# Kernel tuning notes

Hardware: AMD Instinct MI355X
Metric: run time of the kernel (lower is better)

Reference implementation:

```python
import jax, jax.numpy as jnp
import numpy as np


def setup_inputs() -> dict:
    key = jax.random.key(0)
    kx, kq = jax.random.split(key)
    x = jax.random.normal(kx, (64, 1024, 1024), dtype=jnp.float32)
    # K=16 quantization points, sorted (the kernel assumes a fixed ordered set)
    qpoints = jnp.sort(jax.random.uniform(kq, (16,), dtype=jnp.float32,
                                          minval=-1.5, maxval=1.5))
    return {"x": x, "qpoints": qpoints}


def reference(x, qpoints):
    # Nearest-qpoint quantize without materializing an (N, K) distance matrix.
    # searchsorted gives, for each element, the index of the first qpoint >= x;
    # the nearest point is either that one or its left neighbor.
    K = qpoints.shape[0]
    idx = jnp.searchsorted(qpoints, x)            # in [0, K]
    lo = qpoints[jnp.clip(idx - 1, 0, K - 1)]     # left neighbor
    hi = qpoints[jnp.clip(idx, 0, K - 1)]         # right neighbor
    out = jnp.where(jnp.abs(x - lo) <= jnp.abs(x - hi), lo, hi)
    return out
```

## Files before the change

### kernel.cpp

```cpp
#include <hip/hip_runtime.h>


__device__ __forceinline__ float rfl(float v) {
    return __int_as_float(__builtin_amdgcn_readfirstlane(__float_as_int(v)));
}

__device__ __forceinline__ float quant1(float xv, const float qp[16]) {
    float hi = qp[15];
#pragma unroll
    for (int k = 14; k >= 0; --k) hi = (qp[k] >= xv) ? qp[k] : hi;
    float lo = qp[0];
#pragma unroll
    for (int k = 1; k < 16; ++k) lo = (qp[k] < xv) ? qp[k] : lo;
    return (fabsf(xv - lo) <= fabsf(xv - hi)) ? lo : hi;
}

__global__ __launch_bounds__(256) void qquant_vec4(
    const float4* __restrict__ x, const float* __restrict__ q,
    float4* __restrict__ out, int n4) {
    const float4* q4 = (const float4*)q;
    float4 q0 = q4[0], q1 = q4[1], q2 = q4[2], q3 = q4[3];
    float qp[16] = {rfl(q0.x), rfl(q0.y), rfl(q0.z), rfl(q0.w),
                    rfl(q1.x), rfl(q1.y), rfl(q1.z), rfl(q1.w),
                    rfl(q2.x), rfl(q2.y), rfl(q2.z), rfl(q2.w),
                    rfl(q3.x), rfl(q3.y), rfl(q3.z), rfl(q3.w)};

    int stride = gridDim.x * blockDim.x;
    for (int i = blockIdx.x * blockDim.x + threadIdx.x; i < n4; i += stride) {
        float4 v = x[i];
        float4 r;
        r.x = quant1(v.x, qp);
        r.y = quant1(v.y, qp);
        r.z = quant1(v.z, qp);
        r.w = quant1(v.w, qp);
        out[i] = r;
    }
}

__global__ void qquant_tail(const float* __restrict__ x,
                            const float* __restrict__ q,
                            float* __restrict__ out, int start, int n) {
    int i = start + threadIdx.x;
    if (i >= n) return;
    float qp[16];
#pragma unroll
    for (int k = 0; k < 16; ++k) qp[k] = q[k];
    out[i] = quant1(x[i], qp);
}

extern "C" void kernel_launch(void* const* d_in, const int* in_sizes, int n_in,
                              void* d_out, int out_size, void* d_ws, size_t ws_size,
                              hipStream_t stream) {
    const float* x = (const float*)d_in[0];
    const float* q = (const float*)d_in[1];
    float* out = (float*)d_out;
    int n = in_sizes[0];

    int n4 = n >> 2;
    if (n4 > 0) {
        int blocks = (n4 + 255) / 256;
        if (blocks > 8192) blocks = 8192;
        qquant_vec4<<<blocks, 256, 0, stream>>>((const float4*)x, q,
                                                (float4*)out, n4);
    }
    int rem = n & 3;
    if (rem > 0) {
        qquant_tail<<<1, 64, 0, stream>>>(x, q, out, n4 << 2, n);
    }
}
```

Measured before the change: 443.1 us.

## Precompute exact midpoint thresholds and quantize with a single compare chain

Adds a small setup kernel that binary-searches, in ordered-float space, the exact decision threshold between each pair of adjacent qpoints under the reference tie rule, and stores the thresholds in workspace. The main kernel then picks the output with one 15-step compare/select chain per element instead of two 15-step chains plus distance arithmetic. It also switches global loads and stores to nontemporal. This cuts ALU work per element at the cost of an extra tiny kernel launch and a dependence on workspace being available. The kernel is likely near memory-bound, which would limit the benefit.

```diff
diff --git a/kernel.cpp b/kernel.cpp
--- a/kernel.cpp
+++ b/kernel.cpp
@@ -1,8 +1,70 @@
 #include <hip/hip_runtime.h>
 
 
+typedef float f32x4 __attribute__((ext_vector_type(4)));
+
 __device__ __forceinline__ float rfl(float v) {
     return __int_as_float(__builtin_amdgcn_readfirstlane(__float_as_int(v)));
+}
+
+__device__ __forceinline__ unsigned f2o(float f) {
+    unsigned b = __float_as_uint(f);
+    return (b & 0x80000000u) ? ~b : (b | 0x80000000u);
+}
+__device__ __forceinline__ float o2f(unsigned o) {
+    unsigned b = (o & 0x80000000u) ? (o ^ 0x80000000u) : ~o;
+    return __uint_as_float(b);
+}
+
+__global__ void qthresh_setup(const float* __restrict__ q,
+                              float* __restrict__ t) {
+    int k = threadIdx.x;
+    if (k > 15) return;
+    if (k == 15) { t[15] = __uint_as_float(0x7f800000u); return; }
+    float lo = q[k], hi = q[k + 1];
+    unsigned a = f2o(lo), b = f2o(hi);
+    while (b - a > 1u) {
+        unsigned m = a + ((b - a) >> 1);
+        float xm = o2f(m);
+        if (fabsf(xm - lo) <= fabsf(xm - hi)) a = m; else b = m;
+    }
+    t[k] = o2f(a);
+}
+
+__device__ __forceinline__ float chain16(float xv, const float qp[16],
+                                         const float th[15]) {
+    float r = qp[0];
+#pragma unroll
+    for (int k = 0; k < 15; ++k) r = (xv > th[k]) ? qp[k + 1] : r;
+    return r;
+}
+
+__global__ __launch_bounds__(256) void qquant_chain(
+    const f32x4* __restrict__ x, const float* __restrict__ q,
+    const float* __restrict__ t, f32x4* __restrict__ out, int n4) {
+    const f32x4* q4 = (const f32x4*)q;
+    const f32x4* t4 = (const f32x4*)t;
+    f32x4 qa = q4[0], qb = q4[1], qc = q4[2], qd = q4[3];
+    f32x4 ta = t4[0], tb = t4[1], tc = t4[2], td = t4[3];
+    float qp[16] = {rfl(qa.x), rfl(qa.y), rfl(qa.z), rfl(qa.w),
+                    rfl(qb.x), rfl(qb.y), rfl(qb.z), rfl(qb.w),
+                    rfl(qc.x), rfl(qc.y), rfl(qc.z), rfl(qc.w),
+                    rfl(qd.x), rfl(qd.y), rfl(qd.z), rfl(qd.w)};
+    float th[15] = {rfl(ta.x), rfl(ta.y), rfl(ta.z), rfl(ta.w),
+                    rfl(tb.x), rfl(tb.y), rfl(tb.z), rfl(tb.w),
+                    rfl(tc.x), rfl(tc.y), rfl(tc.z), rfl(tc.w),
+                    rfl(td.x), rfl(td.y), rfl(td.z)};
+
+    int stride = gridDim.x * blockDim.x;
+    for (int i = blockIdx.x * blockDim.x + threadIdx.x; i < n4; i += stride) {
+        f32x4 v = __builtin_nontemporal_load(&x[i]);
+        f32x4 r;
+        r.x = chain16(v.x, qp, th);
+        r.y = chain16(v.y, qp, th);
+        r.z = chain16(v.z, qp, th);
+        r.w = chain16(v.w, qp, th);
+        __builtin_nontemporal_store(r, &out[i]);
+    }
 }
 
 __device__ __forceinline__ float quant1(float xv, const float qp[16]) {
@@ -24,7 +86,6 @@
                     rfl(q1.x), rfl(q1.y), rfl(q1.z), rfl(q1.w),
                     rfl(q2.x), rfl(q2.y), rfl(q2.z), rfl(q2.w),
                     rfl(q3.x), rfl(q3.y), rfl(q3.z), rfl(q3.w)};
-
     int stride = gridDim.x * blockDim.x;
     for (int i = blockIdx.x * blockDim.x + threadIdx.x; i < n4; i += stride) {
         float4 v = x[i];
@@ -57,11 +118,19 @@
     int n = in_sizes[0];
 
     int n4 = n >> 2;
+    bool use_ws = (d_ws != nullptr) && (ws_size >= 16 * sizeof(float));
     if (n4 > 0) {
         int blocks = (n4 + 255) / 256;
         if (blocks > 8192) blocks = 8192;
-        qquant_vec4<<<blocks, 256, 0, stream>>>((const float4*)x, q,
-                                                (float4*)out, n4);
+        if (use_ws) {
+            float* t = (float*)d_ws;
+            qthresh_setup<<<1, 64, 0, stream>>>(q, t);
+            qquant_chain<<<blocks, 256, 0, stream>>>((const f32x4*)x, q, t,
+                                                     (f32x4*)out, n4);
+        } else {
+            qquant_vec4<<<blocks, 256, 0, stream>>>((const float4*)x, q,
+                                                    (float4*)out, n4);
+        }
     }
     int rem = n & 3;
     if (rem > 0) {
```

Measured after the change: 450.0 us. No clear change (+1.6%).

## Precompute exact midpoint thresholds per wave and use single compare-select chain

Applied to the files above, without the earlier changes.

Each wave binary-searches, in ordered-integer float space, the exact decision threshold between every pair of adjacent qpoints, reproducing the reference tie-breaking. It broadcasts these thresholds via readlane so each element needs only 15 compare/selects instead of two 15-step chains plus abs/compare. The kernel also processes 8 floats per thread with nontemporal loads and stores. The per-wave binary search adds startup work of up to about 32 iterations, and correctness depends on the qpoints being sorted and on the bit-level search matching the reference rounding.

```diff
diff --git a/kernel.cpp b/kernel.cpp
--- a/kernel.cpp
+++ b/kernel.cpp
@@ -1,8 +1,76 @@
 #include <hip/hip_runtime.h>
 
 
+typedef float f32x4 __attribute__((ext_vector_type(4)));
+
 __device__ __forceinline__ float rfl(float v) {
     return __int_as_float(__builtin_amdgcn_readfirstlane(__float_as_int(v)));
+}
+__device__ __forceinline__ float rdlane(float v, int lane) {
+    return __int_as_float(__builtin_amdgcn_readlane(__float_as_int(v), lane));
+}
+
+__device__ __forceinline__ unsigned f2o(float f) {
+    unsigned b = __float_as_uint(f);
+    return (b & 0x80000000u) ? ~b : (b | 0x80000000u);
+}
+__device__ __forceinline__ float o2f(unsigned o) {
+    unsigned b = (o & 0x80000000u) ? (o ^ 0x80000000u) : ~o;
+    return __uint_as_float(b);
+}
+
+__device__ __forceinline__ float chain16(float xv, const float qp[16],
+                                         const float th[15]) {
+    float r = qp[0];
+#pragma unroll
+    for (int k = 0; k < 15; ++k) r = (xv > th[k]) ? qp[k + 1] : r;
+    return r;
+}
+
+__global__ __launch_bounds__(256) void qquant_fused(
+    const f32x4* __restrict__ x, const float* __restrict__ q,
+    f32x4* __restrict__ out, int n2) {
+    const f32x4* q4 = (const f32x4*)q;
+    f32x4 qa = q4[0], qb = q4[1], qc = q4[2], qd = q4[3];
+    float qp[16] = {rfl(qa.x), rfl(qa.y), rfl(qa.z), rfl(qa.w),
+                    rfl(qb.x), rfl(qb.y), rfl(qb.z), rfl(qb.w),
+                    rfl(qc.x), rfl(qc.y), rfl(qc.z), rfl(qc.w),
+                    rfl(qd.x), rfl(qd.y), rfl(qd.z), rfl(qd.w)};
+
+    int lane = threadIdx.x & 63;
+    float tval = 0.0f;
+    if (lane < 15) {
+        float lo = q[lane], hi = q[lane + 1];
+        unsigned a = f2o(lo), b = f2o(hi);
+        while (b - a > 1u) {
+            unsigned m = a + ((b - a) >> 1);
+            float xm = o2f(m);
+            if (fabsf(xm - lo) <= fabsf(xm - hi)) a = m; else b = m;
+        }
+        tval = o2f(a);
+    }
+    float th[15];
+#pragma unroll
+    for (int j = 0; j < 15; ++j) th[j] = rdlane(tval, j);
+
+    int stride = gridDim.x * blockDim.x;
+    for (int p = blockIdx.x * blockDim.x + threadIdx.x; p < n2; p += stride) {
+        const f32x4* src = &x[2 * p];
+        f32x4 v0 = __builtin_nontemporal_load(&src[0]);
+        f32x4 v1 = __builtin_nontemporal_load(&src[1]);
+        f32x4 r0, r1;
+        r0.x = chain16(v0.x, qp, th);
+        r0.y = chain16(v0.y, qp, th);
+        r0.z = chain16(v0.z, qp, th);
+        r0.w = chain16(v0.w, qp, th);
+        r1.x = chain16(v1.x, qp, th);
+        r1.y = chain16(v1.y, qp, th);
+        r1.z = chain16(v1.z, qp, th);
+        r1.w = chain16(v1.w, qp, th);
+        f32x4* dst = &out[2 * p];
+        __builtin_nontemporal_store(r0, &dst[0]);
+        __builtin_nontemporal_store(r1, &dst[1]);
+    }
 }
 
 __device__ __forceinline__ float quant1(float xv, const float qp[16]) {
@@ -13,28 +81,6 @@
 #pragma unroll
     for (int k = 1; k < 16; ++k) lo = (qp[k] < xv) ? qp[k] : lo;
     return (fabsf(xv - lo) <= fabsf(xv - hi)) ? lo : hi;
-}
-
-__global__ __launch_bounds__(256) void qquant_vec4(
-    const float4* __restrict__ x, const float* __restrict__ q,
-    float4* __restrict__ out, int n4) {
-    const float4* q4 = (const float4*)q;
-    float4 q0 = q4[0], q1 = q4[1], q2 = q4[2], q3 = q4[3];
-    float qp[16] = {rfl(q0.x), rfl(q0.y), rfl(q0.z), rfl(q0.w),
-                    rfl(q1.x), rfl(q1.y), rfl(q1.z), rfl(q1.w),
-                    rfl(q2.x), rfl(q2.y), rfl(q2.z), rfl(q2.w),
-                    rfl(q3.x), rfl(q3.y), rfl(q3.z), rfl(q3.w)};
-
-    int stride = gridDim.x * blockDim.x;
-    for (int i = blockIdx.x * blockDim.x + threadIdx.x; i < n4; i += stride) {
-        float4 v = x[i];
-        float4 r;
-        r.x = quant1(v.x, qp);
-        r.y = quant1(v.y, qp);
-        r.z = quant1(v.z, qp);
-        r.w = quant1(v.w, qp);
-        out[i] = r;
-    }
 }
 
 __global__ void qquant_tail(const float* __restrict__ x,
@@ -56,15 +102,15 @@
     float* out = (float*)d_out;
     int n = in_sizes[0];
 
-    int n4 = n >> 2;
-    if (n4 > 0) {
-        int blocks = (n4 + 255) / 256;
+    int n2 = n >> 3;
+    if (n2 > 0) {
+        int blocks = (n2 + 255) / 256;
         if (blocks > 8192) blocks = 8192;
-        qquant_vec4<<<blocks, 256, 0, stream>>>((const float4*)x, q,
-                                                (float4*)out, n4);
+        qquant_fused<<<blocks, 256, 0, stream>>>((const f32x4*)x, q,
+                                                 (f32x4*)out, n2);
     }
-    int rem = n & 3;
-    if (rem > 0) {
-        qquant_tail<<<1, 64, 0, stream>>>(x, q, out, n4 << 2, n);
+    int done = n2 << 3;
+    if (n - done > 0) {
+        qquant_tail<<<1, 64, 0, stream>>>(x, q, out, done, n);
     }
 }
```

Result: slower. 481.6 us (+8.7%).
